# Kernel optimization log

Measured on AMD Instinct MI355X. Metric: run time of the kernel, lower is better.

## Reference

```python
import jax, jax.numpy as jnp
import numpy as np

TEMP = 0.07


def setup_inputs() -> dict:
    key = jax.random.key(0)
    k1, k2 = jax.random.split(key)
    B, m, d = 256, 128, 768
    v_final = jax.random.normal(k1, (B, d), dtype=jnp.float32)
    T_fused = jax.random.normal(k2, (B, m, d), dtype=jnp.float32)
    return {"v_final": v_final, "T_fused": T_fused}


def reference(v_final, T_fused):
    B = v_final.shape[0]
    # [B, B, m] token-level similarities, scaled by temperature
    sim = jnp.einsum('id,jmd->ijm', v_final, T_fused) / TEMP
    # max over text tokens (ColBERT max-sim) -> [B, B]
    sim_max = sim.max(axis=-1)
    targets = jnp.arange(B)
    # symmetric cross-entropy with diagonal targets
    logp_i2t = jax.nn.log_softmax(sim_max, axis=-1)
    logp_t2i = jax.nn.log_softmax(sim_max.T, axis=-1)
    loss_i2t = -jnp.mean(logp_i2t[targets, targets])
    loss_t2i = -jnp.mean(logp_t2i[targets, targets])
    return (loss_i2t + loss_t2i) / 2
```

## Files before the change

kernel.cpp:

```cpp
#include <hip/hip_runtime.h>
#include <hip/hip_bf16.h>

constexpr int BATCH = 256;
constexpr int MTOK  = 128;
constexpr int DDIM  = 768;
constexpr float INV_TEMP = 1.0f / 0.07f;

typedef __bf16 bf16;
typedef __bf16 bf16x8 __attribute__((ext_vector_type(8)));
typedef float  f32x4  __attribute__((ext_vector_type(4)));

__global__ __launch_bounds__(512, 2) void fused_gemm_max_kernel(
        const float* __restrict__ V,
        const float* __restrict__ T,
        float* __restrict__ S,
        float* __restrict__ ST) {
    __shared__ char  lds[49152];
    __shared__ float smax[256][2];

    const int jt   = blockIdx.x;
    const int tid  = threadIdx.x;
    const int w    = tid >> 6;
    const int lane = tid & 63;
    const int wr   = w >> 1;
    const int wn   = w & 1;
    const int quad = lane >> 4;
    const int l15  = lane & 15;

    const float* gsrc[6];
    int loff[6];
#pragma unroll
    for (int s = 0; s < 6; ++s) {
        int c   = s * 512 + tid;
        int isB = (c >= 2048);
        int cc  = isB ? (c - 2048) : c;
        int row = cc >> 3, kp = cc & 7;
        const float* base = isB ? (T + ((size_t)(jt * MTOK + row)) * DDIM)
                                : (V + (size_t)row * DDIM);
        gsrc[s] = base + kp * 8;
        loff[s] = (isB ? 32768 : 0) + row * 128 + ((kp ^ (row & 7)) << 4);
    }

    int aoff[2][4], boff[2][4];
#pragma unroll
    for (int h = 0; h < 2; ++h)
#pragma unroll
        for (int t = 0; t < 4; ++t) {
            int kp = h * 4 + quad;
            int ar = wr * 64 + t * 16 + l15;
            aoff[h][t] = ar * 128 + ((kp ^ (ar & 7)) << 4);
            int br = wn * 64 + t * 16 + l15;
            boff[h][t] = 32768 + br * 128 + ((kp ^ (br & 7)) << 4);
        }

    f32x4 acc[4][4] = {};

    float4 pre[6][2];
#pragma unroll
    for (int s = 0; s < 6; ++s) {
        pre[s][0] = *(const float4*)(gsrc[s]);
        pre[s][1] = *(const float4*)(gsrc[s] + 4);
    }

    for (int kk = 0; kk < 12; ++kk) {
#pragma unroll
        for (int s = 0; s < 6; ++s) {
            bf16x8 o;
            o[0] = (bf16)pre[s][0].x; o[1] = (bf16)pre[s][0].y;
            o[2] = (bf16)pre[s][0].z; o[3] = (bf16)pre[s][0].w;
            o[4] = (bf16)pre[s][1].x; o[5] = (bf16)pre[s][1].y;
            o[6] = (bf16)pre[s][1].z; o[7] = (bf16)pre[s][1].w;
            *(bf16x8*)(lds + loff[s]) = o;
        }
        __syncthreads();

        if (kk < 11) {
#pragma unroll
            for (int s = 0; s < 6; ++s) {
                const float* p = gsrc[s] + (kk + 1) * 64;
                pre[s][0] = *(const float4*)(p);
                pre[s][1] = *(const float4*)(p + 4);
            }
        }

#pragma unroll
        for (int h = 0; h < 2; ++h) {
            bf16x8 af[4], bb[4];
#pragma unroll
            for (int t = 0; t < 4; ++t) {
                af[t] = *(const bf16x8*)(lds + aoff[h][t]);
                bb[t] = *(const bf16x8*)(lds + boff[h][t]);
            }
#pragma unroll
            for (int tr = 0; tr < 4; ++tr)
#pragma unroll
                for (int tc = 0; tc < 4; ++tc)
                    acc[tr][tc] = __builtin_amdgcn_mfma_f32_16x16x32_bf16(
                        af[tr], bb[tc], acc[tr][tc], 0, 0, 0);
        }
        __syncthreads();
    }

#pragma unroll
    for (int tr = 0; tr < 4; ++tr) {
#pragma unroll
        for (int r = 0; r < 4; ++r) {
            float v = acc[tr][0][r];
            v = fmaxf(v, acc[tr][1][r]);
            v = fmaxf(v, acc[tr][2][r]);
            v = fmaxf(v, acc[tr][3][r]);
            v = fmaxf(v, __shfl_xor(v, 1, 64));
            v = fmaxf(v, __shfl_xor(v, 2, 64));
            v = fmaxf(v, __shfl_xor(v, 4, 64));
            v = fmaxf(v, __shfl_xor(v, 8, 64));
            if (l15 == 0) {
                int row = wr * 64 + tr * 16 + quad * 4 + r;
                smax[row][wn] = v;
            }
        }
    }
    __syncthreads();
    if (tid < BATCH) {
        float v = fmaxf(smax[tid][0], smax[tid][1]) * INV_TEMP;
        S [(size_t)tid * BATCH + jt] = v;
        ST[(size_t)jt  * BATCH + tid] = v;
    }
}

__global__ __launch_bounds__(256) void ce_kernel(
        const float* __restrict__ S,
        const float* __restrict__ ST,
        float* __restrict__ out) {
    const int i = threadIdx.x;
    float mr = -3.4e38f, mc = -3.4e38f;
    for (int j = 0; j < BATCH; ++j) {
        mr = fmaxf(mr, ST[j * BATCH + i]);
        mc = fmaxf(mc, S [j * BATCH + i]);
    }
    float sr = 0.f, sc = 0.f;
    for (int j = 0; j < BATCH; ++j) {
        sr += expf(ST[j * BATCH + i] - mr);
        sc += expf(S [j * BATCH + i] - mc);
    }
    float term = 0.5f * ((mr + logf(sr)) + (mc + logf(sc))) - S[(size_t)i * BATCH + i];

    for (int o = 32; o > 0; o >>= 1) term += __shfl_down(term, o, 64);
    __shared__ float partial[4];
    if ((i & 63) == 0) partial[i >> 6] = term;
    __syncthreads();
    if (i == 0) {
        float t = partial[0] + partial[1] + partial[2] + partial[3];
        out[0] = t / (float)BATCH;
    }
}

extern "C" void kernel_launch(void* const* d_in, const int* in_sizes, int n_in,
                              void* d_out, int out_size, void* d_ws, size_t ws_size,
                              hipStream_t stream) {
    const float* v = (const float*)d_in[0];
    const float* T = (const float*)d_in[1];

    float* S  = (float*)d_ws;
    float* ST = S + BATCH * BATCH;

    fused_gemm_max_kernel<<<256, 512, 0, stream>>>(v, T, S, ST);
    ce_kernel<<<1, 256, 0, stream>>>(S, ST, (float*)d_out);
}
```

Measured before the change: 197.3 us.

## Pre-convert V to bf16, async-load it into LDS, split token tiles, parallelize CE

V is converted to bf16 once in a separate kernel and then streamed into double-buffered LDS with global_load_lds async copies, so each GEMM block no longer re-converts fp32 V. The GEMM grid doubles to 512 blocks of 256 threads, each block handling half the tokens, and writes partial maxima that the CE stage merges. The single-block CE kernel is replaced by a 256-block per-row/column kernel plus a small final reduction. This adds two extra launches and an extra workspace pass over the partial maxima.

```diff
diff --git a/kernel.cpp b/kernel.cpp
--- a/kernel.cpp
+++ b/kernel.cpp
@@ -4,41 +4,63 @@
 constexpr int BATCH = 256;
 constexpr int MTOK  = 128;
 constexpr int DDIM  = 768;
+constexpr int NV    = BATCH * DDIM;
 constexpr float INV_TEMP = 1.0f / 0.07f;
 
 typedef __bf16 bf16;
+typedef __bf16 bf16x4 __attribute__((ext_vector_type(4)));
 typedef __bf16 bf16x8 __attribute__((ext_vector_type(8)));
 typedef float  f32x4  __attribute__((ext_vector_type(4)));
 
-__global__ __launch_bounds__(512, 2) void fused_gemm_max_kernel(
-        const float* __restrict__ V,
+typedef __attribute__((address_space(3))) char       lds_char;
+typedef const __attribute__((address_space(1))) char g_char;
+
+__device__ __forceinline__ void async16(const void* g, void* l) {
+    __builtin_amdgcn_global_load_lds((g_char*)g, (lds_char*)l, 16, 0, 0);
+}
+
+__global__ __launch_bounds__(256) void convert_v_kernel(
+        const float4* __restrict__ v4, bf16x4* __restrict__ out) {
+    int i = blockIdx.x * 256 + threadIdx.x;
+    if (i >= NV / 4) return;
+    float4 f = v4[i];
+    bf16x4 o;
+    o.x = (bf16)f.x; o.y = (bf16)f.y; o.z = (bf16)f.z; o.w = (bf16)f.w;
+    out[i] = o;
+}
+
+__global__ __launch_bounds__(256, 2) void gemm_max_kernel(
+        const bf16*  __restrict__ Vb,
         const float* __restrict__ T,
-        float* __restrict__ S,
-        float* __restrict__ ST) {
-    __shared__ char  lds[49152];
-    __shared__ float smax[256][2];
-
-    const int jt   = blockIdx.x;
+        float* __restrict__ Sp) {
+    __shared__ char  lds[65536 + 8192];
+    __shared__ float smax[256];
+
+    const int jt   = blockIdx.x >> 1;
+    const int mh   = blockIdx.x & 1;
     const int tid  = threadIdx.x;
     const int w    = tid >> 6;
     const int lane = tid & 63;
-    const int wr   = w >> 1;
-    const int wn   = w & 1;
     const int quad = lane >> 4;
     const int l15  = lane & 15;
 
-    const float* gsrc[6];
-    int loff[6];
-#pragma unroll
-    for (int s = 0; s < 6; ++s) {
-        int c   = s * 512 + tid;
-        int isB = (c >= 2048);
-        int cc  = isB ? (c - 2048) : c;
-        int row = cc >> 3, kp = cc & 7;
-        const float* base = isB ? (T + ((size_t)(jt * MTOK + row)) * DDIM)
-                                : (V + (size_t)row * DDIM);
-        gsrc[s] = base + kp * 8;
-        loff[s] = (isB ? 32768 : 0) + row * 128 + ((kp ^ (row & 7)) << 4);
+    const bf16* gA[8];
+#pragma unroll
+    for (int q = 0; q < 8; ++q) {
+        int c = q * 256 + tid;
+        int row = (c >> 2) & 255, sub = c & 3, kh = c >> 10;
+        gA[q] = Vb + (size_t)row * DDIM + kh * 32 + sub * 8;
+    }
+    const int ldsAbase = (tid >> 6) * 1024;
+
+    const float* gB[2];
+    int boffw[2];
+#pragma unroll
+    for (int q = 0; q < 2; ++q) {
+        int c = q * 256 + tid;
+        int row = c >> 3, kp = c & 7;
+        gB[q] = T + (size_t)(jt * MTOK + mh * 64 + row) * DDIM + kp * 8;
+        boffw[q] = 65536 + (kp >> 2) * 4096 + row * 64 + (kp & 3) * 16;
     }
 
     int aoff[2][4], boff[2][4];
@@ -46,40 +68,47 @@
     for (int h = 0; h < 2; ++h)
 #pragma unroll
         for (int t = 0; t < 4; ++t) {
-            int kp = h * 4 + quad;
-            int ar = wr * 64 + t * 16 + l15;
-            aoff[h][t] = ar * 128 + ((kp ^ (ar & 7)) << 4);
-            int br = wn * 64 + t * 16 + l15;
-            boff[h][t] = 32768 + br * 128 + ((kp ^ (br & 7)) << 4);
+            int ar = w * 64 + t * 16 + l15;
+            aoff[h][t] = h * 16384 + ar * 64 + quad * 16;
+            int br = t * 16 + l15;
+            boff[h][t] = 65536 + h * 4096 + br * 64 + quad * 16;
         }
 
     f32x4 acc[4][4] = {};
-
-    float4 pre[6][2];
-#pragma unroll
-    for (int s = 0; s < 6; ++s) {
-        pre[s][0] = *(const float4*)(gsrc[s]);
-        pre[s][1] = *(const float4*)(gsrc[s] + 4);
+    float4 pre[2][2];
+
+#pragma unroll
+    for (int q = 0; q < 8; ++q)
+        async16(gA[q], lds + q * 4096 + ldsAbase);
+#pragma unroll
+    for (int q = 0; q < 2; ++q) {
+        pre[q][0] = *(const float4*)(gB[q]);
+        pre[q][1] = *(const float4*)(gB[q] + 4);
     }
 
     for (int kk = 0; kk < 12; ++kk) {
-#pragma unroll
-        for (int s = 0; s < 6; ++s) {
+        const int buf = (kk & 1) * 32768;
+#pragma unroll
+        for (int q = 0; q < 2; ++q) {
             bf16x8 o;
-            o[0] = (bf16)pre[s][0].x; o[1] = (bf16)pre[s][0].y;
-            o[2] = (bf16)pre[s][0].z; o[3] = (bf16)pre[s][0].w;
-            o[4] = (bf16)pre[s][1].x; o[5] = (bf16)pre[s][1].y;
-            o[6] = (bf16)pre[s][1].z; o[7] = (bf16)pre[s][1].w;
-            *(bf16x8*)(lds + loff[s]) = o;
+            o[0] = (bf16)pre[q][0].x; o[1] = (bf16)pre[q][0].y;
+            o[2] = (bf16)pre[q][0].z; o[3] = (bf16)pre[q][0].w;
+            o[4] = (bf16)pre[q][1].x; o[5] = (bf16)pre[q][1].y;
+            o[6] = (bf16)pre[q][1].z; o[7] = (bf16)pre[q][1].w;
+            *(bf16x8*)(lds + boffw[q]) = o;
         }
         __syncthreads();
 
         if (kk < 11) {
-#pragma unroll
-            for (int s = 0; s < 6; ++s) {
-                const float* p = gsrc[s] + (kk + 1) * 64;
-                pre[s][0] = *(const float4*)(p);
-                pre[s][1] = *(const float4*)(p + 4);
+            const int nbuf = ((kk + 1) & 1) * 32768;
+#pragma unroll
+            for (int q = 0; q < 8; ++q)
+                async16(gA[q] + (kk + 1) * 64, lds + nbuf + q * 4096 + ldsAbase);
+#pragma unroll
+            for (int q = 0; q < 2; ++q) {
+                const float* p = gB[q] + (kk + 1) * 64;
+                pre[q][0] = *(const float4*)(p);
+                pre[q][1] = *(const float4*)(p + 4);
             }
         }
 
@@ -88,7 +117,7 @@
             bf16x8 af[4], bb[4];
 #pragma unroll
             for (int t = 0; t < 4; ++t) {
-                af[t] = *(const bf16x8*)(lds + aoff[h][t]);
+                af[t] = *(const bf16x8*)(lds + buf + aoff[h][t]);
                 bb[t] = *(const bf16x8*)(lds + boff[h][t]);
             }
 #pragma unroll
@@ -113,45 +142,60 @@
             v = fmaxf(v, __shfl_xor(v, 2, 64));
             v = fmaxf(v, __shfl_xor(v, 4, 64));
             v = fmaxf(v, __shfl_xor(v, 8, 64));
-            if (l15 == 0) {
-                int row = wr * 64 + tr * 16 + quad * 4 + r;
-                smax[row][wn] = v;
-            }
+            if (l15 == 0)
+                smax[w * 64 + tr * 16 + quad * 4 + r] = v;
         }
     }
     __syncthreads();
-    if (tid < BATCH) {
-        float v = fmaxf(smax[tid][0], smax[tid][1]) * INV_TEMP;
-        S [(size_t)tid * BATCH + jt] = v;
-        ST[(size_t)jt  * BATCH + tid] = v;
-    }
-}
-
-__global__ __launch_bounds__(256) void ce_kernel(
-        const float* __restrict__ S,
-        const float* __restrict__ ST,
-        float* __restrict__ out) {
+    Sp[(size_t)mh * BATCH * BATCH + (size_t)jt * BATCH + tid] = smax[tid] * INV_TEMP;
+}
+
+__global__ __launch_bounds__(64) void ce1_kernel(
+        const float* __restrict__ Sp, float* __restrict__ partial) {
+    const int t = blockIdx.x;
+    const int l = threadIdx.x;
+    const float* Sp0 = Sp;
+    const float* Sp1 = Sp + BATCH * BATCH;
+
+    float vr[4], vc[4];
+#pragma unroll
+    for (int p = 0; p < 4; ++p) {
+        int j = p * 64 + l;
+        vr[p] = fmaxf(Sp0[j * BATCH + t], Sp1[j * BATCH + t]);
+        int i = p * 64 + l;
+        vc[p] = fmaxf(Sp0[t * BATCH + i], Sp1[t * BATCH + i]);
+    }
+    float mr = fmaxf(fmaxf(vr[0], vr[1]), fmaxf(vr[2], vr[3]));
+    float mc = fmaxf(fmaxf(vc[0], vc[1]), fmaxf(vc[2], vc[3]));
+    for (int o = 32; o > 0; o >>= 1) {
+        mr = fmaxf(mr, __shfl_xor(mr, o, 64));
+        mc = fmaxf(mc, __shfl_xor(mc, o, 64));
+    }
+    float sr = 0.f, sc = 0.f;
+#pragma unroll
+    for (int p = 0; p < 4; ++p) {
+        sr += expf(vr[p] - mr);
+        sc += expf(vc[p] - mc);
+    }
+    for (int o = 32; o > 0; o >>= 1) {
+        sr += __shfl_xor(sr, o, 64);
+        sc += __shfl_xor(sc, o, 64);
+    }
+    if (l == 0) {
+        float diag = fmaxf(Sp0[t * BATCH + t], Sp1[t * BATCH + t]);
+        partial[t] = 0.5f * ((mr + logf(sr)) + (mc + logf(sc))) - diag;
+    }
+}
+
+__global__ __launch_bounds__(256) void ce2_kernel(
+        const float* __restrict__ partial, float* __restrict__ out) {
     const int i = threadIdx.x;
-    float mr = -3.4e38f, mc = -3.4e38f;
-    for (int j = 0; j < BATCH; ++j) {
-        mr = fmaxf(mr, ST[j * BATCH + i]);
-        mc = fmaxf(mc, S [j * BATCH + i]);
-    }
-    float sr = 0.f, sc = 0.f;
-    for (int j = 0; j < BATCH; ++j) {
-        sr += expf(ST[j * BATCH + i] - mr);
-        sc += expf(S [j * BATCH + i] - mc);
-    }
-    float term = 0.5f * ((mr + logf(sr)) + (mc + logf(sc))) - S[(size_t)i * BATCH + i];
-
+    float term = partial[i];
     for (int o = 32; o > 0; o >>= 1) term += __shfl_down(term, o, 64);
-    __shared__ float partial[4];
-    if ((i & 63) == 0) partial[i >> 6] = term;
+    __shared__ float ps[4];
+    if ((i & 63) == 0) ps[i >> 6] = term;
     __syncthreads();
-    if (i == 0) {
-        float t = partial[0] + partial[1] + partial[2] + partial[3];
-        out[0] = t / (float)BATCH;
-    }
+    if (i == 0) out[0] = (ps[0] + ps[1] + ps[2] + ps[3]) / (float)BATCH;
 }
 
 extern "C" void kernel_launch(void* const* d_in, const int* in_sizes, int n_in,
@@ -160,9 +204,13 @@
     const float* v = (const float*)d_in[0];
     const float* T = (const float*)d_in[1];
 
-    float* S  = (float*)d_ws;
-    float* ST = S + BATCH * BATCH;
-
-    fused_gemm_max_kernel<<<256, 512, 0, stream>>>(v, T, S, ST);
-    ce_kernel<<<1, 256, 0, stream>>>(S, ST, (float*)d_out);
-}
+    bf16*  Vb = (bf16*)d_ws;
+    float* Sp = (float*)((char*)d_ws + (size_t)NV * sizeof(bf16));
+    float* partial = Sp + 2 * BATCH * BATCH;
+
+    convert_v_kernel<<<(NV / 4 + 255) / 256, 256, 0, stream>>>(
+        (const float4*)v, (bf16x4*)Vb);
+    gemm_max_kernel<<<512, 256, 0, stream>>>(Vb, T, Sp);
+    ce1_kernel<<<256, 64, 0, stream>>>(Sp, partial);
+    ce2_kernel<<<1, 256, 0, stream>>>(partial, (float*)d_out);
+}
```

Result: faster. 168.9 us (-14.4%).
